# Optimization experiments

Measured on AMD Instinct MI355X. Metric: run time of the kernel, lower is better.

## Reference

```python
import jax, jax.numpy as jnp
from jax import lax
import numpy as np

DN = ('NCHW', 'OIHW', 'NCHW')
COMMIT = 0.25
K, D = 512, 64

def conv(x, w, b, s, p):
    y = lax.conv_general_dilated(x, w, (s, s), [(p, p), (p, p)], dimension_numbers=DN)
    return y + b[None, :, None, None]

def convT(x, w, b, s, p):
    # torch ConvTranspose2d weight layout (in, out, kh, kw) -> flip + swap to OIHW
    wf = jnp.flip(w, (2, 3)).transpose(1, 0, 2, 3)
    q = w.shape[2] - 1 - p
    y = lax.conv_general_dilated(x, wf, (1, 1), [(q, q), (q, q)], lhs_dilation=(s, s), dimension_numbers=DN)
    return y + b[None, :, None, None]

def res_stack(x, blocks):
    # ResidualLayer: x + Conv1x1(ReLU(Conv3x3(ReLU(x)))); final ReLU after stack
    for wa, ba, wb, bb in blocks:
        x = x + conv(jax.nn.relu(conv(jax.nn.relu(x), wa, ba, 1, 1)), wb, bb, 1, 0)
    return jax.nn.relu(x)

def setup_inputs():
    key = jax.random.key(0)
    ks = iter(jax.random.split(key, 64))
    def rn(shape, scale=0.05):
        return jax.random.normal(next(ks), shape, jnp.float32) * scale
    z = lambda *s: jnp.zeros(s, jnp.float32)
    return dict(
        x=jax.random.uniform(next(ks), (16, 5, 256, 256), jnp.float32),
        taylor_c=jnp.array([0.0, 1.0, 0.05, 0.01, 0.001], jnp.float32),
        ca_w1=rn((4, 5)), ca_b1=z(4), ca_w2=rn((5, 4)), ca_b2=z(5),
        sa_w=rn((1, 2, 7, 7)), sa_b=z(1),
        mix_w=rn((3, 5, 1, 1), 0.3), mix_b=z(3),
        bn_g=jnp.ones(3, jnp.float32), bn_b=z(3), bn_m=z(3), bn_v=jnp.ones(3, jnp.float32),
        e1_w=rn((64, 3, 4, 4)), e1_b=z(64),
        e2_w=rn((128, 64, 4, 4)), e2_b=z(128),
        e3_w=rn((128, 128, 3, 3)), e3_b=z(128),
        er1a_w=rn((32, 128, 3, 3)), er1a_b=z(32), er1b_w=rn((128, 32, 1, 1)), er1b_b=z(128),
        er2a_w=rn((32, 128, 3, 3)), er2a_b=z(32), er2b_w=rn((128, 32, 1, 1)), er2b_b=z(128),
        ep_w=rn((64, 128, 1, 1)), ep_b=z(64),
        codebook=jax.random.uniform(next(ks), (K, D), jnp.float32, -1.0 / K, 1.0 / K),
        d1_w=rn((64, 128, 3, 3)), d1_b=z(128),
        dr1a_w=rn((32, 128, 3, 3)), dr1a_b=z(32), dr1b_w=rn((128, 32, 1, 1)), dr1b_b=z(128),
        dr2a_w=rn((32, 128, 3, 3)), dr2a_b=z(32), dr2b_w=rn((128, 32, 1, 1)), dr2b_b=z(128),
        d2_w=rn((128, 64, 4, 4)), d2_b=z(64),
        d3_w=rn((64, 5, 4, 4)), d3_b=z(5),
    )

def reference(x, taylor_c, ca_w1, ca_b1, ca_w2, ca_b2, sa_w, sa_b, mix_w, mix_b, bn_g, bn_b, bn_m, bn_v, e1_w, e1_b, e2_w, e2_b, e3_w, e3_b, er1a_w, er1a_b, er1b_w, er1b_b, er2a_w, er2a_b, er2b_w, er2b_b, ep_w, ep_b, codebook, d1_w, d1_b, dr1a_w, dr1a_b, dr1b_w, dr1b_b, dr2a_w, dr2a_b, dr2b_w, dr2b_b, d2_w, d2_b, d3_w, d3_b):
    # ---- AE_TSCM ----
    c = taylor_c
    t = c[0] + c[1] * x + c[2] * x**2 / 2 + c[3] * x**3 / 6 + c[4] * x**4 / 24
    gap = t.mean((2, 3))  # (B, C)
    chw = jax.nn.sigmoid(jax.nn.relu(gap @ ca_w1.T + ca_b1) @ ca_w2.T + ca_b2)
    t = t * chw[:, :, None, None]
    sp_in = jnp.concatenate([t.mean(1, keepdims=True), t.max(1, keepdims=True)], axis=1)
    t = t * jax.nn.sigmoid(conv(sp_in, sa_w, sa_b, 1, 3))
    t = conv(t, mix_w, mix_b, 1, 0)
    t = (t - bn_m[None, :, None, None]) * (bn_g / jnp.sqrt(bn_v + 1e-5))[None, :, None, None] + bn_b[None, :, None, None]
    t = jnp.where(t >= 0, t, 0.1 * t)  # LeakyReLU(0.1)
    mn = t.min((2, 3), keepdims=True)
    mx = t.max((2, 3), keepdims=True)
    t = (t - mn) / (mx - mn + 1e-4)  # ChannelNormalize
    # ---- Encoder ----
    h = jax.nn.relu(conv(t, e1_w, e1_b, 2, 1))
    h = jax.nn.relu(conv(h, e2_w, e2_b, 2, 1))
    h = conv(h, e3_w, e3_b, 1, 1)
    h = res_stack(h, [(er1a_w, er1a_b, er1b_w, er1b_b), (er2a_w, er2a_b, er2b_w, er2b_b)])
    zenc = conv(h, ep_w, ep_b, 1, 0)  # (B, D, 64, 64)
    # ---- VQ-EMA (eval forward) ----
    zp = zenc.transpose(0, 2, 3, 1)  # BHWC
    zf = zp.reshape(-1, D)
    dist = (zf**2).sum(1, keepdims=True) + (codebook**2).sum(1) - 2.0 * zf @ codebook.T
    idx = jnp.argmin(dist, axis=1)
    q = codebook[idx].reshape(zp.shape)
    vq_loss = COMMIT * jnp.mean((zp - lax.stop_gradient(q))**2)
    q_st = zp + lax.stop_gradient(q - zp)  # straight-through
    counts = jnp.zeros((K,), zf.dtype).at[idx].add(1.0)
    avg_probs = counts / zf.shape[0]
    perplexity = jnp.exp(-jnp.sum(avg_probs * jnp.log(avg_probs + 1e-10)))
    zq = q_st.transpose(0, 3, 1, 2)
    # ---- Decoder ----
    h = convT(zq, d1_w, d1_b, 1, 1)
    h = res_stack(h, [(dr1a_w, dr1a_b, dr1b_w, dr1b_b), (dr2a_w, dr2a_b, dr2b_w, dr2b_b)])
    h = jax.nn.relu(convT(h, d2_w, d2_b, 2, 1))
    recon = convT(h, d3_w, d3_b, 2, 1)  # (B, 5, 256, 256)
    return recon, vq_loss, perplexity
```

## Files before the change

### kernel.cpp

```cpp
#include <hip/hip_runtime.h>

#define DEV __device__ __forceinline__

typedef float f4_t __attribute__((ext_vector_type(4)));

DEV unsigned f2ord(float f){ unsigned u=__float_as_uint(f); return (u&0x80000000u)? ~u : (u|0x80000000u); }
DEV float ord2f(unsigned o){ unsigned u=(o&0x80000000u)? (o&0x7FFFFFFFu) : ~o; return __uint_as_float(u); }
DEV float wsum(float v){ for(int o=32;o;o>>=1) v+=__shfl_down(v,o,64); return v; }
DEV float wminr(float v){ for(int o=32;o;o>>=1) v=fminf(v,__shfl_down(v,o,64)); return v; }
DEV float wmaxr(float v){ for(int o=32;o;o>>=1) v=fmaxf(v,__shfl_down(v,o,64)); return v; }

__global__ void k_init(float* counts, unsigned* mnmx){
  int i = threadIdx.x;
  if (i < 512) counts[i] = 0.f;
  if (i < 48) mnmx[i] = 0xFFFFFFFFu;
  if (i >= 64 && i < 112) mnmx[i-64+48] = 0u;
}

__global__ __launch_bounds__(256) void k_taylor(const float* __restrict__ x, const float* __restrict__ tc,
                                                float* __restrict__ t, float* __restrict__ gpart){
  int blk = blockIdx.x;
  int bc = blk >> 6, chunk = blk & 63;
  float k0=tc[0], k1=tc[1], k2=tc[2]*0.5f, k3=tc[3]*(1.f/6.f), k4=tc[4]*(1.f/24.f);
  size_t base = (size_t)bc*65536 + (size_t)chunk*1024;
  float s = 0.f;
  #pragma unroll
  for (int j=0;j<4;j++){
    size_t i = base + threadIdx.x + j*256;
    float xv = x[i];
    float tv = k0 + xv*(k1 + xv*(k2 + xv*(k3 + xv*k4)));
    t[i] = tv; s += tv;
  }
  s = wsum(s);
  __shared__ float ws4[4];
  int lane = threadIdx.x & 63, wv = threadIdx.x >> 6;
  if (lane==0) ws4[wv]=s;
  __syncthreads();
  if (threadIdx.x==0) gpart[blk] = ws4[0]+ws4[1]+ws4[2]+ws4[3];
}

__global__ void k_chw(const float* __restrict__ gpart, const float* __restrict__ w1, const float* __restrict__ b1,
                      const float* __restrict__ w2, const float* __restrict__ b2,
                      const float* __restrict__ bng, const float* __restrict__ bnb,
                      const float* __restrict__ bnm, const float* __restrict__ bnv,
                      float* __restrict__ chw, float* __restrict__ bnsb){
  __shared__ float g[80];
  int tid = threadIdx.x;
  if (tid < 80){
    float s = 0.f;
    for (int j=0;j<64;j++) s += gpart[tid*64+j];
    g[tid] = s * (1.f/65536.f);
  }
  __syncthreads();
  if (tid < 16){
    int b = tid;
    float h[4];
    for (int j=0;j<4;j++){
      float a = b1[j];
      for (int c=0;c<5;c++) a += g[b*5+c]*w1[j*5+c];
      h[j] = fmaxf(a, 0.f);
    }
    for (int c=0;c<5;c++){
      float a = b2[c];
      for (int j=0;j<4;j++) a += h[j]*w2[c*4+j];
      chw[b*5+c] = 1.f/(1.f+expf(-a));
    }
  } else if (tid >= 32 && tid < 35){
    int c = tid-32;
    float sc = bng[c] / sqrtf(bnv[c] + 1e-5f);
    bnsb[c] = sc;
    bnsb[4+c] = bnb[c] - bnm[c]*sc;
  }
}

__global__ __launch_bounds__(256) void k_spin(float* __restrict__ t, const float* __restrict__ chw,
                                              float* __restrict__ spm, float* __restrict__ spx){
  int b = blockIdx.y;
  int p = blockIdx.x*256 + threadIdx.x;
  size_t base = ((size_t)b*5)*65536 + p;
  float vs=0.f, vmax=-3.0e38f;
  #pragma unroll
  for (int c=0;c<5;c++){
    float v = t[base + (size_t)c*65536] * chw[b*5+c];
    t[base + (size_t)c*65536] = v;
    vs += v; vmax = fmaxf(vmax, v);
  }
  spm[(size_t)b*65536+p] = vs*0.2f;
  spx[(size_t)b*65536+p] = vmax;
}

__global__ __launch_bounds__(256) void k_sa(const float* __restrict__ spm, const float* __restrict__ spx,
                                            const float* __restrict__ w, const float* __restrict__ bias,
                                            float* __restrict__ samap){
  int b = blockIdx.y;
  int p = blockIdx.x*256 + threadIdx.x;
  int y0 = p >> 8, x0 = p & 255;
  float acc = bias[0];
  const float* sp0 = spm + (size_t)b*65536;
  const float* sp1 = spx + (size_t)b*65536;
  #pragma unroll
  for (int ky=0;ky<7;ky++){
    int iy = y0 - 3 + ky;
    if ((unsigned)iy >= 256u) continue;
    #pragma unroll
    for (int kx=0;kx<7;kx++){
      int ix = x0 - 3 + kx;
      if ((unsigned)ix >= 256u) continue;
      acc += sp0[iy*256+ix] * w[ky*7+kx] + sp1[iy*256+ix] * w[49+ky*7+kx];
    }
  }
  samap[(size_t)b*65536+p] = 1.f/(1.f+expf(-acc));
}

__global__ __launch_bounds__(256) void k_mix(const float* __restrict__ t, const float* __restrict__ samap,
                                             const float* __restrict__ mw, const float* __restrict__ mb,
                                             const float* __restrict__ bnsb, float* __restrict__ t3,
                                             unsigned* __restrict__ mnmx){
  int b = blockIdx.y;
  int p = blockIdx.x*256 + threadIdx.x;
  float s = samap[(size_t)b*65536+p];
  float v[5];
  #pragma unroll
  for (int c=0;c<5;c++) v[c] = t[((size_t)b*5+c)*65536+p] * s;
  float mn[3], mx[3];
  #pragma unroll
  for (int co=0;co<3;co++){
    float a = mb[co];
    #pragma unroll
    for (int ci=0;ci<5;ci++) a += v[ci]*mw[co*5+ci];
    a = a*bnsb[co] + bnsb[4+co];
    a = (a >= 0.f) ? a : 0.1f*a;
    t3[((size_t)b*3+co)*65536+p] = a;
    mn[co]=a; mx[co]=a;
  }
  __shared__ float smn[3][4], smx[3][4];
  int lane = threadIdx.x & 63, wv = threadIdx.x >> 6;
  #pragma unroll
  for (int co=0;co<3;co++){
    float lmn = wminr(mn[co]);
    float lmx = wmaxr(mx[co]);
    if (lane==0){ smn[co][wv]=lmn; smx[co][wv]=lmx; }
  }
  __syncthreads();
  if (threadIdx.x==0){
    #pragma unroll
    for (int co=0;co<3;co++){
      float m0 = fminf(fminf(smn[co][0],smn[co][1]),fminf(smn[co][2],smn[co][3]));
      float m1 = fmaxf(fmaxf(smx[co][0],smx[co][1]),fmaxf(smx[co][2],smx[co][3]));
      atomicMin(&mnmx[b*3+co], f2ord(m0));
      atomicMax(&mnmx[48+b*3+co], f2ord(m1));
    }
  }
}

__global__ __launch_bounds__(256) void k_norm(float* __restrict__ t3, const unsigned* __restrict__ mnmx){
  int i = blockIdx.x*256 + threadIdx.x;
  int bc = i >> 16;
  float mn = ord2f(mnmx[bc]);
  float mx = ord2f(mnmx[48+bc]);
  t3[i] = (t3[i] - mn) / (mx - mn + 1e-4f);
}

__global__ void k_pack(const float* __restrict__ w, float* __restrict__ wt, int CIN, int COUT, int KHW){
  int i = blockIdx.x*256 + threadIdx.x;
  int total = CIN*COUT*KHW;
  if (i >= total) return;
  int co = i % COUT; int tt = i / COUT;
  int ci = tt / KHW, k = tt % KHW;
  wt[i] = w[(co*CIN + ci)*KHW + k];
}
__global__ void k_pack_d1(const float* __restrict__ w, float* __restrict__ wt){
  int i = blockIdx.x*256 + threadIdx.x;
  if (i >= 64*9*128) return;
  int co = i & 127; int tt = i >> 7;
  int ci = tt / 9, k = tt % 9;
  int ky = k/3, kx = k%3;
  wt[i] = w[(ci*128 + co)*9 + (2-ky)*3 + (2-kx)];
}
__global__ void k_pack_d2p(const float* __restrict__ w, float* __restrict__ wt){
  int i = blockIdx.x*256 + threadIdx.x;
  if (i >= 131072) return;
  int co = i & 63; int t = i >> 6;
  int kk = t & 3; int t2 = t >> 2;
  int ci = t2 & 127; int par = t2 >> 7;
  int py = par >> 1, px = par & 1;
  int kyp = kk >> 1, kxp = kk & 1;
  int ky = 3 - py - 2*kyp;
  int kx = 3 - px - 2*kxp;
  wt[i] = w[((size_t)ci*64 + co)*16 + ky*4 + kx];
}
__global__ void k_pack_d3p(const float* __restrict__ w, float* __restrict__ wt){
  int i = blockIdx.x*256 + threadIdx.x;
  if (i >= 5120) return;
  int co = i % 5; int t = i / 5;
  int kk = t & 3; int t2 = t >> 2;
  int ci = t2 & 63; int par = t2 >> 6;
  int py = par >> 1, px = par & 1;
  int kyp = kk >> 1, kxp = kk & 1;
  int ky = 3 - py - 2*kyp;
  int kx = 3 - px - 2*kxp;
  wt[i] = w[((size_t)ci*5 + co)*16 + ky*4 + kx];
}
__global__ void k_cb2(const float* __restrict__ cb, float* __restrict__ cb2){
  int c = blockIdx.x*64 + threadIdx.x;
  if (c >= 512) return;
  float s=0.f;
  for (int d=0; d<64; d++){ float v = cb[c*64+d]; s += v*v; }
  cb2[c] = s;
}

template<int CIN,int COUT,int KH,int KW,int S,int P,bool RIN,bool ROUT,bool ADD>
__global__ __launch_bounds__(256) void convk(const float* __restrict__ x, const float* __restrict__ wt,
                                             const float* __restrict__ bias, const float* __restrict__ res,
                                             float* __restrict__ y, int HIN, int WIN, int HOUT, int WOUT){
  int p = blockIdx.x*256 + threadIdx.x;
  int npix = HOUT*WOUT;
  if (p >= npix) return;
  int oy = p / WOUT, ox = p - oy*WOUT;
  int co = blockIdx.y*4;
  int n = blockIdx.z;
  const float* xn = x + (size_t)n*CIN*HIN*WIN;
  float a0=bias[co], a1=bias[co+1], a2=bias[co+2], a3=bias[co+3];
  #pragma unroll
  for (int ky=0; ky<KH; ky++){
    int iy = oy*S - P + ky;
    bool rok = (unsigned)iy < (unsigned)HIN;
    #pragma unroll
    for (int kx=0; kx<KW; kx++){
      int ix = ox*S - P + kx;
      bool ok = rok && ((unsigned)ix < (unsigned)WIN);
      const float* xp = xn + (size_t)iy*WIN + ix;
      const float* wp = wt + (ky*KW + kx)*COUT + co;
      #pragma unroll 4
      for (int ci=0; ci<CIN; ci++){
        float v = ok ? xp[(size_t)ci*HIN*WIN] : 0.f;
        if (RIN) v = fmaxf(v, 0.f);
        const float4 w4 = *reinterpret_cast<const float4*>(wp + ci*KH*KW*COUT);
        a0 = fmaf(v, w4.x, a0);
        a1 = fmaf(v, w4.y, a1);
        a2 = fmaf(v, w4.z, a2);
        a3 = fmaf(v, w4.w, a3);
      }
    }
  }
  if (ROUT){ a0=fmaxf(a0,0.f); a1=fmaxf(a1,0.f); a2=fmaxf(a2,0.f); a3=fmaxf(a3,0.f); }
  size_t yb = ((size_t)n*COUT + co)*npix + p;
  if (ADD){
    a0 += res[yb]; a1 += res[yb+(size_t)npix]; a2 += res[yb+(size_t)2*npix]; a3 += res[yb+(size_t)3*npix];
  }
  y[yb] = a0; y[yb+(size_t)npix] = a1; y[yb+(size_t)2*npix] = a2; y[yb+(size_t)3*npix] = a3;
}

template<int CIN,int COUT,int KH,int KW,int PY,int PX,int ROWS,int U,bool RIN,bool ROUT,bool ADD>
__global__ __launch_bounds__(256) void conv8(const float* __restrict__ x, const float* __restrict__ wt,
                                             const float* __restrict__ bias, const float* __restrict__ res,
                                             float* __restrict__ y,
                                             int plane, int rstr, int cstr, int obase){
  constexpr int KHW = KH*KW;
  constexpr int NR  = KH + ROWS - 1;
  int tid = threadIdx.x;
  int cob = blockIdx.y*8;
  int ox  = tid & 63;
  int oy0 = blockIdx.x*(4*ROWS) + (tid>>6)*ROWS;
  int n   = blockIdx.z;
  const float* xn = x + (size_t)n*CIN*4096;
  f4_t b0 = *(const f4_t*)&bias[cob];
  f4_t b1 = *(const f4_t*)&bias[cob+4];
  f4_t acc0[ROWS], acc1[ROWS];
  #pragma unroll
  for (int r=0;r<ROWS;r++){ acc0[r] = b0; acc1[r] = b1; }

  for (int cb0=0; cb0<CIN; cb0+=U){
    #pragma unroll
    for (int u=0; u<U; u++){
      int ci = cb0 + u;
      const float* xc = xn + (size_t)ci*4096;
      float c0[NR], cl[NR], cr[NR];
      #pragma unroll
      for (int rr=0; rr<NR; rr++){
        int iy = oy0 - PY + rr;
        bool vr = (unsigned)iy < 64u;
        float v = vr ? xc[iy*64 + ox] : 0.f;
        if (RIN) v = fmaxf(v, 0.f);
        c0[rr] = v;
      }
      #pragma unroll
      for (int rr=0; rr<NR; rr++){
        if (KW == 3){
          float l = __shfl_up(c0[rr], 1, 64);   if (ox==0)  l = 0.f;
          float g = __shfl_down(c0[rr], 1, 64); if (ox==63) g = 0.f;
          cl[rr] = l; cr[rr] = g;
        } else if (KW == 2){
          float s;
          if (PX == 1){ s = __shfl_up(c0[rr], 1, 64);   if (ox==0)  s = 0.f; }
          else        { s = __shfl_down(c0[rr], 1, 64); if (ox==63) s = 0.f; }
          cl[rr] = s;
        }
      }
      const float* wci = wt + (size_t)ci*KHW*COUT + cob;
      #pragma unroll
      for (int ky=0; ky<KH; ky++){
        #pragma unroll
        for (int kx=0; kx<KW; kx++){
          f4_t w0 = *(const f4_t*)(wci + (ky*KW + kx)*COUT);
          f4_t w1 = *(const f4_t*)(wci + (ky*KW + kx)*COUT + 4);
          #pragma unroll
          for (int r=0; r<ROWS; r++){
            int rr = r + ky;
            float v;
            if (KW == 1)      v = c0[rr];
            else if (KW == 3) v = (kx==0) ? cl[rr] : ((kx==1) ? c0[rr] : cr[rr]);
            else              v = (kx==PX) ? c0[rr] : cl[rr];
            acc0[r] += v * w0;
            acc1[r] += v * w1;
          }
        }
      }
    }
  }

  #pragma unroll
  for (int r=0;r<ROWS;r++){
    size_t base = ((size_t)n*COUT + cob)*plane + (size_t)(oy0+r)*rstr + obase + ox*cstr;
    #pragma unroll
    for (int j=0;j<8;j++){
      float a = (j<4) ? ((const float*)&acc0[r])[j] : ((const float*)&acc1[r])[j-4];
      if (ROUT) a = fmaxf(a, 0.f);
      if (ADD)  a += res[base + (size_t)j*plane];
      y[base + (size_t)j*plane] = a;
    }
  }
}

template<int CIN,int COUT,int ROWS,bool RIN,bool ROUT>
__global__ __launch_bounds__(256) void conv8s2(const float* __restrict__ x, const float* __restrict__ wt,
                                               const float* __restrict__ bias, float* __restrict__ y){
  constexpr int NRI = 2*ROWS + 2;
  int tid = threadIdx.x;
  int cob = blockIdx.y*8;
  int ox  = tid & 63;
  int oy0 = blockIdx.x*(4*ROWS) + (tid>>6)*ROWS;
  int n   = blockIdx.z;
  const float* xn = x + (size_t)n*CIN*16384;
  f4_t b0 = *(const f4_t*)&bias[cob];
  f4_t b1 = *(const f4_t*)&bias[cob+4];
  f4_t acc0[ROWS], acc1[ROWS];
  #pragma unroll
  for (int r=0;r<ROWS;r++){ acc0[r] = b0; acc1[r] = b1; }

  #pragma unroll 2
  for (int ci=0; ci<CIN; ci++){
    const float* xc = xn + (size_t)ci*16384;
    float A[NRI], Bb[NRI], L[NRI], R[NRI];
    #pragma unroll
    for (int rr=0; rr<NRI; rr++){
      int iy = 2*oy0 - 1 + rr;
      bool vr = (unsigned)iy < 128u;
      float a = 0.f, b = 0.f;
      if (vr){
        float2 ab = *(const float2*)(xc + iy*128 + 2*ox);
        a = ab.x; b = ab.y;
      }
      if (RIN){ a = fmaxf(a,0.f); b = fmaxf(b,0.f); }
      A[rr] = a; Bb[rr] = b;
    }
    #pragma unroll
    for (int rr=0; rr<NRI; rr++){
      float l = __shfl_up(Bb[rr], 1, 64);  if (ox==0)  l = 0.f;
      float g = __shfl_down(A[rr], 1, 64); if (ox==63) g = 0.f;
      L[rr] = l; R[rr] = g;
    }
    const float* wci = wt + (size_t)ci*16*COUT + cob;
    #pragma unroll
    for (int ky=0; ky<4; ky++){
      #pragma unroll
      for (int kx=0; kx<4; kx++){
        f4_t w0 = *(const f4_t*)(wci + (ky*4 + kx)*COUT);
        f4_t w1 = *(const f4_t*)(wci + (ky*4 + kx)*COUT + 4);
        #pragma unroll
        for (int r=0; r<ROWS; r++){
          int rr = 2*r + ky;
          float v = (kx==0) ? L[rr] : ((kx==1) ? A[rr] : ((kx==2) ? Bb[rr] : R[rr]));
          acc0[r] += v * w0;
          acc1[r] += v * w1;
        }
      }
    }
  }

  #pragma unroll
  for (int r=0;r<ROWS;r++){
    size_t base = ((size_t)n*COUT + cob)*4096 + (size_t)(oy0+r)*64 + ox;
    #pragma unroll
    for (int j=0;j<8;j++){
      float a = (j<4) ? ((const float*)&acc0[r])[j] : ((const float*)&acc1[r])[j-4];
      if (ROUT) a = fmaxf(a, 0.f);
      y[base + (size_t)j*4096] = a;
    }
  }
}

__global__ __launch_bounds__(256) void convd2(const float* __restrict__ x, const float* __restrict__ wt,
                                              const float* __restrict__ bias, float* __restrict__ y){
  constexpr int ROWS = 4;
  constexpr int NR   = ROWS + 1;
  int par  = blockIdx.y >> 3;
  int cob  = (blockIdx.y & 7)*8;
  int py   = par >> 1, px = par & 1;
  int PY   = 1 - py,  PX = 1 - px;
  int obase = py*128 + px;
  const float* wpar = wt + par*32768;
  int tid = threadIdx.x;
  int ox  = tid & 63;
  int oy0 = blockIdx.x*(4*ROWS) + (tid>>6)*ROWS;
  int n   = blockIdx.z;
  const float* xn = x + (size_t)n*128*4096;
  f4_t b0 = *(const f4_t*)&bias[cob];
  f4_t b1 = *(const f4_t*)&bias[cob+4];
  f4_t acc0[ROWS], acc1[ROWS];
  #pragma unroll
  for (int r=0;r<ROWS;r++){ acc0[r] = b0; acc1[r] = b1; }

  #pragma unroll 2
  for (int ci=0; ci<128; ci++){
    const float* xc = xn + (size_t)ci*4096;
    float c0[NR], cl[NR];
    #pragma unroll
    for (int rr=0; rr<NR; rr++){
      int iy = oy0 - PY + rr;
      bool vr = (unsigned)iy < 64u;
      float v = vr ? xc[iy*64 + ox] : 0.f;
      v = fmaxf(v, 0.f);
      c0[rr] = v;
    }
    if (PX == 1){
      #pragma unroll
      for (int rr=0; rr<NR; rr++){
        float su = __shfl_up(c0[rr], 1, 64); if (ox==0) su = 0.f;
        cl[rr] = su;
      }
    } else {
      #pragma unroll
      for (int rr=0; rr<NR; rr++){
        float sd = __shfl_down(c0[rr], 1, 64); if (ox==63) sd = 0.f;
        cl[rr] = sd;
      }
    }
    const float* wci = wpar + (size_t)ci*4*64 + cob;
    #pragma unroll
    for (int ky=0; ky<2; ky++){
      #pragma unroll
      for (int kx=0; kx<2; kx++){
        f4_t w0 = *(const f4_t*)(wci + (ky*2 + kx)*64);
        f4_t w1 = *(const f4_t*)(wci + (ky*2 + kx)*64 + 4);
        #pragma unroll
        for (int r=0; r<ROWS; r++){
          int rr = r + ky;
          float v = (kx == PX) ? c0[rr] : cl[rr];
          acc0[r] += v * w0;
          acc1[r] += v * w1;
        }
      }
    }
  }

  #pragma unroll
  for (int r=0;r<ROWS;r++){
    size_t base = ((size_t)n*64 + cob)*16384 + (size_t)(oy0+r)*256 + obase + ox*2;
    #pragma unroll
    for (int j=0;j<8;j++){
      float a = (j<4) ? ((const float*)&acc0[r])[j] : ((const float*)&acc1[r])[j-4];
      a = fmaxf(a, 0.f);
      y[base + (size_t)j*16384] = a;
    }
  }
}

__global__ __launch_bounds__(256) void convd3(const float* __restrict__ x, const float* __restrict__ wt,
                                              const float* __restrict__ bias, float* __restrict__ y){
  constexpr int ROWS = 2;
  constexpr int NRI  = ROWS + 1;
  int par  = blockIdx.y;
  int py   = par >> 1, px = par & 1;
  int PY   = 1 - py,  PX = 1 - px;
  const float* wpar = wt + par*1280;
  int tid  = threadIdx.x;
  int lane = tid & 63, wv = tid >> 6;
  int oy0  = blockIdx.x*(4*ROWS) + wv*ROWS;
  int n    = blockIdx.z;
  const float* xn = x + (size_t)n*64*16384;
  float b[5];
  #pragma unroll
  for (int j=0;j<5;j++) b[j] = bias[j];
  float acc[ROWS][2][5];
  #pragma unroll
  for (int r=0;r<ROWS;r++)
    #pragma unroll
    for (int c=0;c<2;c++)
      #pragma unroll
      for (int j=0;j<5;j++) acc[r][c][j] = b[j];

  #pragma unroll 2
  for (int ci=0; ci<64; ci++){
    const float* xc = xn + (size_t)ci*16384;
    float A[NRI], Bv[NRI], S[NRI];
    #pragma unroll
    for (int rr=0; rr<NRI; rr++){
      int iy = oy0 - PY + rr;
      float a = 0.f, bb = 0.f;
      if ((unsigned)iy < 128u){
        float2 ab = *(const float2*)(xc + iy*128 + 2*lane);
        a = ab.x; bb = ab.y;
      }
      A[rr] = a; Bv[rr] = bb;
    }
    if (PX == 1){
      #pragma unroll
      for (int rr=0; rr<NRI; rr++){
        float l = __shfl_up(Bv[rr], 1, 64); if (lane==0) l = 0.f;
        S[rr] = l;
      }
    } else {
      #pragma unroll
      for (int rr=0; rr<NRI; rr++){
        float g = __shfl_down(A[rr], 1, 64); if (lane==63) g = 0.f;
        S[rr] = g;
      }
    }
    const float* wci = wpar + ci*20;
    #pragma unroll
    for (int kyp=0; kyp<2; kyp++){
      #pragma unroll
      for (int kxp=0; kxp<2; kxp++){
        const float* wp = wci + (kyp*2 + kxp)*5;
        #pragma unroll
        for (int r=0; r<ROWS; r++){
          int rr = r + kyp;
          float v0, v1;
          if (PX == 1){ v0 = (kxp==0) ? S[rr]  : A[rr];  v1 = (kxp==0) ? A[rr]  : Bv[rr]; }
          else        { v0 = (kxp==0) ? A[rr]  : Bv[rr]; v1 = (kxp==0) ? Bv[rr] : S[rr];  }
          #pragma unroll
          for (int j=0;j<5;j++){
            acc[r][0][j] = fmaf(v0, wp[j], acc[r][0][j]);
            acc[r][1][j] = fmaf(v1, wp[j], acc[r][1][j]);
          }
        }
      }
    }
  }

  #pragma unroll
  for (int r=0;r<ROWS;r++){
    size_t rowb = (size_t)n*5*65536 + (size_t)(2*(oy0+r)+py)*256;
    #pragma unroll
    for (int j=0;j<5;j++){
      y[rowb + (size_t)j*65536 + 4*lane + px]     = acc[r][0][j];
      y[rowb + (size_t)j*65536 + 4*lane + 2 + px] = acc[r][1][j];
    }
  }
}

__global__ __launch_bounds__(256) void k_vq(const float* __restrict__ zenc, const float* __restrict__ cb,
                                            const float* __restrict__ cb2, int* __restrict__ idx,
                                            float* __restrict__ lossp, float* __restrict__ counts){
  int r = blockIdx.x*256 + threadIdx.x;
  int b = r >> 12, p = r & 4095;
  const float* zp = zenc + ((size_t)b*64)*4096 + p;
  float z[64];
  float z2 = 0.f;
  #pragma unroll
  for (int d=0; d<64; d++){ z[d] = zp[(size_t)d*4096]; z2 += z[d]*z[d]; }
  float best = 3.4e38f; int bi = 0;
  for (int c=0; c<512; c+=4){
    float dot0=0.f, dot1=0.f, dot2=0.f, dot3=0.f;
    const float* c0 = cb + c*64;
    #pragma unroll
    for (int d=0; d<64; d++){
      float zd = z[d];
      dot0 = fmaf(zd, c0[d],     dot0);
      dot1 = fmaf(zd, c0[64+d],  dot1);
      dot2 = fmaf(zd, c0[128+d], dot2);
      dot3 = fmaf(zd, c0[192+d], dot3);
    }
    float d0 = (z2 + cb2[c])   - 2.f*dot0;
    float d1 = (z2 + cb2[c+1]) - 2.f*dot1;
    float d2 = (z2 + cb2[c+2]) - 2.f*dot2;
    float d3 = (z2 + cb2[c+3]) - 2.f*dot3;
    if (d0 < best){ best = d0; bi = c; }
    if (d1 < best){ best = d1; bi = c+1; }
    if (d2 < best){ best = d2; bi = c+2; }
    if (d3 < best){ best = d3; bi = c+3; }
  }
  idx[r] = bi;
  float l = 0.f;
  const float* cbest = cb + bi*64;
  #pragma unroll
  for (int d=0; d<64; d++){ float df = z[d]-cbest[d]; l = fmaf(df,df,l); }
  l = wsum(l);
  __shared__ float ls[4];
  __shared__ int hist[512];
  int lane = threadIdx.x & 63, wv = threadIdx.x >> 6;
  if (lane==0) ls[wv] = l;
  for (int i=threadIdx.x; i<512; i+=256) hist[i]=0;
  __syncthreads();
  atomicAdd(&hist[bi], 1);
  if (threadIdx.x==0) lossp[blockIdx.x] = ls[0]+ls[1]+ls[2]+ls[3];
  __syncthreads();
  for (int i=threadIdx.x; i<512; i+=256){
    int h = hist[i];
    if (h) atomicAdd(&counts[i], (float)h);
  }
}

__global__ void k_finalize(const float* __restrict__ counts, const float* __restrict__ lossp,
                           float* __restrict__ out){
  __shared__ float sl[8], st[8];
  int tid = threadIdx.x;
  int lane = tid & 63, wv = tid >> 6;
  float lp = (tid < 256) ? lossp[tid] : 0.f;
  lp = wsum(lp);
  if (lane==0) sl[wv] = lp;
  float pr = counts[tid] * (1.f/65536.f);
  float term = pr * logf(pr + 1e-10f);
  term = wsum(term);
  if (lane==0) st[wv] = term;
  __syncthreads();
  if (tid==0){
    float L=0.f, S=0.f;
    for (int i=0;i<8;i++){ L += sl[i]; S += st[i]; }
    out[5242880] = L * 0.25f / (65536.f*64.f);
    out[5242881] = expf(-S);
  }
}

__global__ __launch_bounds__(256) void k_gather(const float* __restrict__ cb, const int* __restrict__ idx,
                                                float* __restrict__ zq){
  int i = blockIdx.x*256 + threadIdx.x;
  int p = i & 4095;
  int d = (i >> 12) & 63;
  int b = i >> 18;
  zq[i] = cb[idx[(b<<12) + p]*64 + d];
}

extern "C" void kernel_launch(void* const* d_in, const int* in_sizes, int n_in,
                              void* d_out, int out_size, void* d_ws, size_t ws_size,
                              hipStream_t stream){
  (void)in_sizes; (void)n_in; (void)out_size;
  const float* x     = (const float*)d_in[0];
  const float* tc    = (const float*)d_in[1];
  const float* ca_w1 = (const float*)d_in[2];
  const float* ca_b1 = (const float*)d_in[3];
  const float* ca_w2 = (const float*)d_in[4];
  const float* ca_b2 = (const float*)d_in[5];
  const float* sa_w  = (const float*)d_in[6];
  const float* sa_b  = (const float*)d_in[7];
  const float* mix_w = (const float*)d_in[8];
  const float* mix_b = (const float*)d_in[9];
  const float* bn_g  = (const float*)d_in[10];
  const float* bn_b  = (const float*)d_in[11];
  const float* bn_m  = (const float*)d_in[12];
  const float* bn_v  = (const float*)d_in[13];
  const float* e1_w  = (const float*)d_in[14];
  const float* e1_b  = (const float*)d_in[15];
  const float* e2_w  = (const float*)d_in[16];
  const float* e2_b  = (const float*)d_in[17];
  const float* e3_w  = (const float*)d_in[18];
  const float* e3_b  = (const float*)d_in[19];
  const float* er1a_w= (const float*)d_in[20];
  const float* er1a_b= (const float*)d_in[21];
  const float* er1b_w= (const float*)d_in[22];
  const float* er1b_b= (const float*)d_in[23];
  const float* er2a_w= (const float*)d_in[24];
  const float* er2a_b= (const float*)d_in[25];
  const float* er2b_w= (const float*)d_in[26];
  const float* er2b_b= (const float*)d_in[27];
  const float* ep_w  = (const float*)d_in[28];
  const float* ep_b  = (const float*)d_in[29];
  const float* cb    = (const float*)d_in[30];
  const float* d1_w  = (const float*)d_in[31];
  const float* d1_b  = (const float*)d_in[32];
  const float* dr1a_w= (const float*)d_in[33];
  const float* dr1a_b= (const float*)d_in[34];
  const float* dr1b_w= (const float*)d_in[35];
  const float* dr1b_b= (const float*)d_in[36];
  const float* dr2a_w= (const float*)d_in[37];
  const float* dr2a_b= (const float*)d_in[38];
  const float* dr2b_w= (const float*)d_in[39];
  const float* dr2b_b= (const float*)d_in[40];
  const float* d2_w  = (const float*)d_in[41];
  const float* d2_b  = (const float*)d_in[42];
  const float* d3_w  = (const float*)d_in[43];
  const float* d3_b  = (const float*)d_in[44];
  float* out = (float*)d_out;
  float* ws = (float*)d_ws;

  size_t o = 0;
  auto alloc = [&](size_t n){ size_t r = o; o += (n + 63) & ~63ull; return r; };
  size_t f_buf0 = alloc(16777216);
  size_t f_buf1 = alloc(8388608);
  size_t f_buf2 = alloc(8388608);
  size_t f_buf3 = alloc(5242880);
  size_t f_buf4 = alloc(3145728);
  size_t f_spm  = alloc(1048576);
  size_t f_spx  = alloc(1048576);
  size_t f_sam  = alloc(1048576);
  size_t f_gpart= alloc(5120);
  size_t f_chw  = alloc(80);
  size_t f_bnsb = alloc(8);
  size_t f_mnmx = alloc(96);
  size_t f_counts=alloc(512);
  size_t f_lossp= alloc(256);
  size_t f_cb2  = alloc(512);
  size_t f_idx  = alloc(65536);
  size_t f_wt_e1= alloc(3072);
  size_t f_wt_e2= alloc(131072);
  size_t f_wt_e3= alloc(147456);
  size_t f_wt_ra1=alloc(36864);
  size_t f_wt_rb1=alloc(4096);
  size_t f_wt_ra2=alloc(36864);
  size_t f_wt_rb2=alloc(4096);
  size_t f_wt_ep= alloc(8192);
  size_t f_wt_d1= alloc(73728);
  size_t f_wt_da1=alloc(36864);
  size_t f_wt_db1=alloc(4096);
  size_t f_wt_da2=alloc(36864);
  size_t f_wt_db2=alloc(4096);
  size_t f_wt_d2= alloc(131072);
  size_t f_wt_d3= alloc(5120);
  if (ws_size < o*sizeof(float)) return;

  float* t    = ws + f_buf3;
  float* zenc = ws + f_buf3;
  float* h1   = ws + f_buf0;
  float* zq   = ws + f_buf0;
  float* dh2  = ws + f_buf0;
  float* h2   = ws + f_buf1;
  float* dh1  = ws + f_buf1;
  float* h3   = ws + f_buf2;
  float* t3   = ws + f_buf4;
  float* spm  = ws + f_spm;
  float* spx  = ws + f_spx;
  float* rtmp = ws + f_spm;
  float* samap= ws + f_sam;
  unsigned* mnmx = (unsigned*)(ws + f_mnmx);
  int* idx = (int*)(ws + f_idx);

  dim3 T(256);

  k_init<<<1, 512, 0, stream>>>(ws + f_counts, mnmx);

  k_pack<<<(3072+255)/256, T, 0, stream>>>(e1_w, ws+f_wt_e1, 3, 64, 16);
  k_pack<<<(131072+255)/256, T, 0, stream>>>(e2_w, ws+f_wt_e2, 64, 128, 16);
  k_pack<<<(147456+255)/256, T, 0, stream>>>(e3_w, ws+f_wt_e3, 128, 128, 9);
  k_pack<<<(36864+255)/256, T, 0, stream>>>(er1a_w, ws+f_wt_ra1, 128, 32, 9);
  k_pack<<<(4096+255)/256, T, 0, stream>>>(er1b_w, ws+f_wt_rb1, 32, 128, 1);
  k_pack<<<(36864+255)/256, T, 0, stream>>>(er2a_w, ws+f_wt_ra2, 128, 32, 9);
  k_pack<<<(4096+255)/256, T, 0, stream>>>(er2b_w, ws+f_wt_rb2, 32, 128, 1);
  k_pack<<<(8192+255)/256, T, 0, stream>>>(ep_w, ws+f_wt_ep, 128, 64, 1);
  k_pack_d1<<<(73728+255)/256, T, 0, stream>>>(d1_w, ws+f_wt_d1);
  k_pack<<<(36864+255)/256, T, 0, stream>>>(dr1a_w, ws+f_wt_da1, 128, 32, 9);
  k_pack<<<(4096+255)/256, T, 0, stream>>>(dr1b_w, ws+f_wt_db1, 32, 128, 1);
  k_pack<<<(36864+255)/256, T, 0, stream>>>(dr2a_w, ws+f_wt_da2, 128, 32, 9);
  k_pack<<<(4096+255)/256, T, 0, stream>>>(dr2b_w, ws+f_wt_db2, 32, 128, 1);
  k_pack_d2p<<<512, T, 0, stream>>>(d2_w, ws+f_wt_d2);
  k_pack_d3p<<<20, T, 0, stream>>>(d3_w, ws+f_wt_d3);
  k_cb2<<<8, 64, 0, stream>>>(cb, ws+f_cb2);

  k_taylor<<<5120, T, 0, stream>>>(x, tc, t, ws+f_gpart);
  k_chw<<<1, 128, 0, stream>>>(ws+f_gpart, ca_w1, ca_b1, ca_w2, ca_b2, bn_g, bn_b, bn_m, bn_v,
                               ws+f_chw, ws+f_bnsb);
  k_spin<<<dim3(256,16), T, 0, stream>>>(t, ws+f_chw, spm, spx);
  k_sa<<<dim3(256,16), T, 0, stream>>>(spm, spx, sa_w, sa_b, samap);
  k_mix<<<dim3(256,16), T, 0, stream>>>(t, samap, mix_w, mix_b, ws+f_bnsb, t3, mnmx);
  k_norm<<<12288, T, 0, stream>>>(t3, mnmx);

  convk<3,64,4,4,2,1,false,true,false><<<dim3(64,16,16), T, 0, stream>>>(t3, ws+f_wt_e1, e1_b, nullptr, h1, 256,256,128,128);
  conv8s2<64,128,2,false,true><<<dim3(8,16,16), T, 0, stream>>>(h1, ws+f_wt_e2, e2_b, h2);
  conv8<128,128,3,3,1,1,4,2,false,false,false><<<dim3(4,16,16), T, 0, stream>>>(h2, ws+f_wt_e3, e3_b, nullptr, h3, 4096,64,1,0);
  conv8<128,32,3,3,1,1,1,2,true,true,false><<<dim3(16,4,16), T, 0, stream>>>(h3, ws+f_wt_ra1, er1a_b, nullptr, rtmp, 4096,64,1,0);
  conv8<32,128,1,1,0,0,2,4,false,false,true><<<dim3(8,16,16), T, 0, stream>>>(rtmp, ws+f_wt_rb1, er1b_b, h3, h3, 4096,64,1,0);
  conv8<128,32,3,3,1,1,1,2,true,true,false><<<dim3(16,4,16), T, 0, stream>>>(h3, ws+f_wt_ra2, er2a_b, nullptr, rtmp, 4096,64,1,0);
  conv8<32,128,1,1,0,0,2,4,false,false,true><<<dim3(8,16,16), T, 0, stream>>>(rtmp, ws+f_wt_rb2, er2b_b, h3, h3, 4096,64,1,0);
  conv8<128,64,1,1,0,0,2,4,true,false,false><<<dim3(8,8,16), T, 0, stream>>>(h3, ws+f_wt_ep, ep_b, nullptr, zenc, 4096,64,1,0);

  k_vq<<<256, T, 0, stream>>>(zenc, cb, ws+f_cb2, idx, ws+f_lossp, ws+f_counts);
  k_finalize<<<1, 512, 0, stream>>>(ws+f_counts, ws+f_lossp, out);
  k_gather<<<16384, T, 0, stream>>>(cb, idx, zq);

  conv8<64,128,3,3,1,1,4,2,false,false,false><<<dim3(4,16,16), T, 0, stream>>>(zq, ws+f_wt_d1, d1_b, nullptr, dh1, 4096,64,1,0);
  conv8<128,32,3,3,1,1,1,2,true,true,false><<<dim3(16,4,16), T, 0, stream>>>(dh1, ws+f_wt_da1, dr1a_b, nullptr, rtmp, 4096,64,1,0);
  conv8<32,128,1,1,0,0,2,4,false,false,true><<<dim3(8,16,16), T, 0, stream>>>(rtmp, ws+f_wt_db1, dr1b_b, dh1, dh1, 4096,64,1,0);
  conv8<128,32,3,3,1,1,1,2,true,true,false><<<dim3(16,4,16), T, 0, stream>>>(dh1, ws+f_wt_da2, dr2a_b, nullptr, rtmp, 4096,64,1,0);
  conv8<32,128,1,1,0,0,2,4,false,false,true><<<dim3(8,16,16), T, 0, stream>>>(rtmp, ws+f_wt_db2, dr2b_b, dh1, dh1, 4096,64,1,0);
  convd2<<<dim3(4,32,16), T, 0, stream>>>(dh1, ws+f_wt_d2, d2_b, dh2);
  convd3<<<dim3(16,4,16), T, 0, stream>>>(dh2, ws+f_wt_d3, d3_b, out);
}
```

Baseline: 2.439 ms.

## Split VQ codebook scan across four blocks with 64-bit atomicMin merge

The VQ nearest-code search now runs as a 256x4 grid, with each block scanning a quarter of the codebook. Per-row partial minima are merged through a packed (ordered distance, index) 64-bit atomicMin into a keys buffer that a new init kernel sets beforehand. A separate finalize kernel reads the winning index, recomputes the loss from zenc, and builds the histogram. The original 256-block launch badly underfilled the GPU; the split adds two extra launches, extra zenc reads and atomics. Ties now resolve to the lowest index across quarters, which is consistent with argmin.

```diff
diff --git a/kernel.cpp b/kernel.cpp
--- a/kernel.cpp
+++ b/kernel.cpp
@@ -15,6 +15,10 @@
   if (i < 512) counts[i] = 0.f;
   if (i < 48) mnmx[i] = 0xFFFFFFFFu;
   if (i >= 64 && i < 112) mnmx[i-64+48] = 0u;
+}
+__global__ void k_initvq(unsigned long long* keys){
+  int i = blockIdx.x*256 + threadIdx.x;
+  keys[i] = ~0ull;
 }
 
 __global__ __launch_bounds__(256) void k_taylor(const float* __restrict__ x, const float* __restrict__ tc,
@@ -560,10 +564,11 @@
   }
 }
 
-__global__ __launch_bounds__(256) void k_vq(const float* __restrict__ zenc, const float* __restrict__ cb,
-                                            const float* __restrict__ cb2, int* __restrict__ idx,
-                                            float* __restrict__ lossp, float* __restrict__ counts){
+__global__ __launch_bounds__(256) void k_vqscan(const float* __restrict__ zenc, const float* __restrict__ cb,
+                                                const float* __restrict__ cb2,
+                                                unsigned long long* __restrict__ keys){
   int r = blockIdx.x*256 + threadIdx.x;
+  int q = blockIdx.y;
   int b = r >> 12, p = r & 4095;
   const float* zp = zenc + ((size_t)b*64)*4096 + p;
   float z[64];
@@ -571,7 +576,8 @@
   #pragma unroll
   for (int d=0; d<64; d++){ z[d] = zp[(size_t)d*4096]; z2 += z[d]*z[d]; }
   float best = 3.4e38f; int bi = 0;
-  for (int c=0; c<512; c+=4){
+  int cbeg = q*128;
+  for (int c=cbeg; c<cbeg+128; c+=4){
     float dot0=0.f, dot1=0.f, dot2=0.f, dot3=0.f;
     const float* c0 = cb + c*64;
     #pragma unroll
@@ -591,11 +597,23 @@
     if (d2 < best){ best = d2; bi = c+2; }
     if (d3 < best){ best = d3; bi = c+3; }
   }
+  unsigned long long key = ((unsigned long long)f2ord(best) << 32) | (unsigned long long)(unsigned)bi;
+  atomicMin(&keys[r], key);
+}
+
+__global__ __launch_bounds__(256) void k_vqfin(const float* __restrict__ zenc, const float* __restrict__ cb,
+                                               const unsigned long long* __restrict__ keys,
+                                               int* __restrict__ idx, float* __restrict__ lossp,
+                                               float* __restrict__ counts){
+  int r = blockIdx.x*256 + threadIdx.x;
+  int b = r >> 12, p = r & 4095;
+  int bi = (int)(keys[r] & 0xFFFFFFFFull);
   idx[r] = bi;
+  const float* zp = zenc + ((size_t)b*64)*4096 + p;
+  const float* cbest = cb + bi*64;
   float l = 0.f;
-  const float* cbest = cb + bi*64;
-  #pragma unroll
-  for (int d=0; d<64; d++){ float df = z[d]-cbest[d]; l = fmaf(df,df,l); }
+  #pragma unroll
+  for (int d=0; d<64; d++){ float df = zp[(size_t)d*4096] - cbest[d]; l = fmaf(df,df,l); }
   l = wsum(l);
   __shared__ float ls[4];
   __shared__ int hist[512];
@@ -712,6 +730,7 @@
   size_t f_lossp= alloc(256);
   size_t f_cb2  = alloc(512);
   size_t f_idx  = alloc(65536);
+  size_t f_vqkey= alloc(131072);
   size_t f_wt_e1= alloc(3072);
   size_t f_wt_e2= alloc(131072);
   size_t f_wt_e3= alloc(147456);
@@ -744,10 +763,12 @@
   float* samap= ws + f_sam;
   unsigned* mnmx = (unsigned*)(ws + f_mnmx);
   int* idx = (int*)(ws + f_idx);
+  unsigned long long* vqkeys = (unsigned long long*)(ws + f_vqkey);
 
   dim3 T(256);
 
   k_init<<<1, 512, 0, stream>>>(ws + f_counts, mnmx);
+  k_initvq<<<256, T, 0, stream>>>(vqkeys);
 
   k_pack<<<(3072+255)/256, T, 0, stream>>>(e1_w, ws+f_wt_e1, 3, 64, 16);
   k_pack<<<(131072+255)/256, T, 0, stream>>>(e2_w, ws+f_wt_e2, 64, 128, 16);
@@ -783,7 +804,8 @@
   conv8<32,128,1,1,0,0,2,4,false,false,true><<<dim3(8,16,16), T, 0, stream>>>(rtmp, ws+f_wt_rb2, er2b_b, h3, h3, 4096,64,1,0);
   conv8<128,64,1,1,0,0,2,4,true,false,false><<<dim3(8,8,16), T, 0, stream>>>(h3, ws+f_wt_ep, ep_b, nullptr, zenc, 4096,64,1,0);
 
-  k_vq<<<256, T, 0, stream>>>(zenc, cb, ws+f_cb2, idx, ws+f_lossp, ws+f_counts);
+  k_vqscan<<<dim3(256,4), T, 0, stream>>>(zenc, cb, ws+f_cb2, vqkeys);
+  k_vqfin<<<256, T, 0, stream>>>(zenc, cb, vqkeys, idx, ws+f_lossp, ws+f_counts);
   k_finalize<<<1, 512, 0, stream>>>(ws+f_counts, ws+f_lossp, out);
   k_gather<<<16384, T, 0, stream>>>(cb, idx, zq);
 
```

After: 2.257 ms. 1.08x faster.
